# Performance work log

Hardware: AMD Instinct MI355X
Metric: run time of the kernel (lower is better)

## Reference

```python
import jax, jax.numpy as jnp
import numpy as np
import math

B, T, M, C, H = 2, 2048, 1024, 512, 8
D = C // H  # head dim = 64


def setup_inputs() -> dict:
    key = jax.random.key(0)
    ks = jax.random.split(key, 6)
    return {
        "x": jax.random.normal(ks[0], (B, T, C), jnp.float32),
        "y": jax.random.normal(ks[1], (B, M, C), jnp.float32),
        "attn_x_mask": jnp.ones((1, 1, T, T), jnp.int32),
        "qkv_w": jax.random.normal(ks[2], (3 * C, C), jnp.float32) * 0.02,
        "qkv_b": jax.random.normal(ks[3], (3 * C,), jnp.float32) * 0.02,
        "proj_w": jax.random.normal(ks[4], (C, C), jnp.float32) * 0.02,
        "proj_b": jax.random.normal(ks[5], (C,), jnp.float32) * 0.02,
    }


def _split_heads(t, n, d):
    # [B, N, C] -> [B, H, N, D]
    b = t.shape[0]
    return t.reshape(b, n, H, d).transpose(0, 2, 1, 3)


def reference(x, y, attn_x_mask, qkv_w, qkv_b, proj_w, proj_b):
    b, t, c = x.shape
    m = y.shape[1]
    d = c // H
    scale = 1.0 / math.sqrt(d)

    # shared qkv projection applied to x and y (torch Linear: x @ W.T + b)
    qkv_x = x @ qkv_w.T + qkv_b
    q_x, k_x, v_x = jnp.split(qkv_x, 3, axis=-1)
    qkv_y = y @ qkv_w.T + qkv_b
    q_y, k_y, v_y = jnp.split(qkv_y, 3, axis=-1)

    q_x, k_x, v_x = (_split_heads(a, t, d) for a in (q_x, k_x, v_x))
    q_y, k_y, v_y = (_split_heads(a, m, d) for a in (q_y, k_y, v_y))

    # x -> y cross attention scores (pre-softmax, reused for chaining)
    catt_x2y = jnp.einsum("bhtd,bhmd->bhtm", q_x, k_y) * scale  # [B,H,T,M]
    cval_x2y = jnp.einsum("bhtm,bhmd->bhtd", jax.nn.softmax(catt_x2y, axis=-1), v_y)
    cval_x2y = cval_x2y.transpose(0, 2, 1, 3).reshape(b, t, c)

    # y -> x scores, then chained through raw x2y scores
    catt_y2x = jnp.einsum("bhmd,bhsd->bhms", q_y, k_x) * scale  # [B,H,M,T]
    chained = jnp.einsum("bhtm,bhms->bhts", catt_x2y, catt_y2x) * scale  # [B,H,T,T]
    chained = jnp.where(attn_x_mask == 0, -jnp.inf, chained)
    cval_y2x = jnp.einsum("bhts,bhsd->bhtd", jax.nn.softmax(chained, axis=-1), v_x)
    cval_y2x = cval_y2x.transpose(0, 2, 1, 3).reshape(b, t, c)

    out = cval_x2y - cval_y2x
    out = out @ proj_w.T + proj_b  # dropout layers are identity in eval mode
    return out
```

## Files before the change

### kernel.cpp

```cpp
#include <hip/hip_runtime.h>


typedef _Float16 half_t;
typedef _Float16 half8 __attribute__((ext_vector_type(8)));
typedef _Float16 half4v __attribute__((ext_vector_type(4)));
typedef float floatx4 __attribute__((ext_vector_type(4)));
typedef int int4v __attribute__((ext_vector_type(4)));

constexpr int Bc = 2, Tc = 2048, Mc = 1024, Cc = 512, Hc = 8, Dc = 64;
constexpr long BTC = (long)Bc * Tc * Cc;
constexpr long ZT  = (long)Bc * Hc * Tc;
constexpr float S1 = 0.18033688f;

enum { EPI_F16STORE = 0, EPI_QKV_XY = 1, EPI_PROJ = 2 };

struct EpiParams {
  half_t* h0;
  half_t* h1;
  half_t* h2;
  half_t* h3;
  half_t* h4;
  half_t* h5;
  half_t* h6;
  float* f0;
  const float* bias;
  float scale;
  int ldc;
  long bstride;
};

__device__ __forceinline__ void gld_lds16(const half_t* g, half_t* l) {
  __builtin_amdgcn_global_load_lds(
      (const __attribute__((address_space(1))) void*)g,
      (__attribute__((address_space(3))) void*)l, 16, 0, 0);
}

__device__ __forceinline__ int pkrtz(float a, float b) {
  return __builtin_bit_cast(int, __builtin_amdgcn_cvt_pkrtz(a, b));
}
__device__ __forceinline__ void pl16(int& a, int& b) {
  asm volatile("v_permlane16_swap_b32 %0, %1" : "+v"(a), "+v"(b));
}
__device__ __forceinline__ void pl32(int& a, int& b) {
  asm volatile("v_permlane32_swap_b32 %0, %1" : "+v"(a), "+v"(b));
}

template <int BM, int BN, int WMG, int WNG, int EPI>
__global__ __launch_bounds__(256) void gemm_nt(
    const half_t* __restrict__ A, const half_t* __restrict__ Bt,
    int K, int lda, int ldb, long bsA, long bsB, EpiParams ep)
{
  constexpr int BK = 64;
  constexpr int WTM = BM / WMG, WTN = BN / WNG;
  constexpr int MI = WTM / 16, NI = WTN / 16;
  constexpr int AIT = BM * BK / 8 / 256;
  constexpr int BIT = BN * BK / 8 / 256;
  constexpr int NLD = AIT + BIT;
  __shared__ __align__(16) half_t As[2][BM * BK];
  __shared__ __align__(16) half_t Bs[2][BN * BK];

  const int tid = threadIdx.x;
  const int lane = tid & 63;
  const int wave = tid >> 6;
  const int wm = wave / WNG, wn = wave % WNG;
  const int r16 = lane & 15, g = lane >> 4;
  const int z = blockIdx.z;
  const long m0 = (long)blockIdx.y * BM;
  const long n0 = (long)blockIdx.x * BN;
  const half_t* Abase = A + (long)z * bsA + m0 * (long)lda;
  const half_t* Bbase = Bt + (long)z * bsB + n0 * (long)ldb;

  const int rA = wm * WTM + r16;
  const int rB = wn * WTN + r16;

  floatx4 acc[MI][NI];
#pragma unroll
  for (int mi = 0; mi < MI; ++mi)
#pragma unroll
    for (int ni = 0; ni < NI; ++ni)
      acc[mi][ni] = floatx4{0.f, 0.f, 0.f, 0.f};

  auto stage = [&](int kt, int buf) {
#pragma unroll
    for (int i = 0; i < AIT; ++i) {
      const int c = tid + i * 256;
      const int row = c >> 3, js = c & 7;
      const int jg = js ^ (row & 7);
      gld_lds16(Abase + (long)row * lda + kt + jg * 8, &As[buf][c * 8]);
    }
#pragma unroll
    for (int i = 0; i < BIT; ++i) {
      const int c = tid + i * 256;
      const int row = c >> 3, js = c & 7;
      const int jg = js ^ (row & 7);
      gld_lds16(Bbase + (long)row * ldb + kt + jg * 8, &Bs[buf][c * 8]);
    }
  };

  const int NIT = K / BK;
  stage(0, 0);
  asm volatile("" ::: "memory");

  for (int it = 0; it < NIT; ++it) {
    const bool hn = (it + 1 < NIT);
    if (hn) stage((it + 1) * BK, (it + 1) & 1);
    asm volatile("" ::: "memory");
    if (hn) {
      if constexpr (NLD == 6) asm volatile("s_waitcnt vmcnt(6)" ::: "memory");
      else if constexpr (NLD == 4) asm volatile("s_waitcnt vmcnt(4)" ::: "memory");
      else if constexpr (NLD == 8) asm volatile("s_waitcnt vmcnt(8)" ::: "memory");
      else asm volatile("s_waitcnt vmcnt(0)" ::: "memory");
    } else {
      asm volatile("s_waitcnt vmcnt(0)" ::: "memory");
    }
    __builtin_amdgcn_s_barrier();
    asm volatile("" ::: "memory");

    const half_t* Ab = As[it & 1];
    const half_t* Bb = Bs[it & 1];
    half8 aF[MI][2], bF[NI][2];
#pragma unroll
    for (int mi = 0; mi < MI; ++mi)
#pragma unroll
      for (int k2 = 0; k2 < 2; ++k2)
        aF[mi][k2] = *reinterpret_cast<const half8*>(
            &Ab[(rA + mi * 16) * BK + ((k2 * 4 + g) ^ (r16 & 7)) * 8]);
#pragma unroll
    for (int ni = 0; ni < NI; ++ni)
#pragma unroll
      for (int k2 = 0; k2 < 2; ++k2)
        bF[ni][k2] = *reinterpret_cast<const half8*>(
            &Bb[(rB + ni * 16) * BK + ((k2 * 4 + g) ^ (r16 & 7)) * 8]);
    __builtin_amdgcn_s_setprio(1);
#pragma unroll
    for (int k2 = 0; k2 < 2; ++k2)
#pragma unroll
      for (int mi = 0; mi < MI; ++mi)
#pragma unroll
        for (int ni = 0; ni < NI; ++ni)
          acc[mi][ni] = __builtin_amdgcn_mfma_f32_16x16x32_f16(
              aF[mi][k2], bF[ni][k2], acc[mi][ni], 0, 0, 0);
    __builtin_amdgcn_s_setprio(0);
    asm volatile("s_waitcnt lgkmcnt(0)" ::: "memory");
    __builtin_amdgcn_s_barrier();
    asm volatile("" ::: "memory");
  }

#pragma unroll
  for (int mi = 0; mi < MI; ++mi) {
#pragma unroll
    for (int ni = 0; ni < NI; ++ni) {
#pragma unroll
      for (int reg = 0; reg < 4; ++reg) {
        const int r = (int)m0 + wm * WTM + mi * 16 + g * 4 + reg;
        const int c = (int)n0 + wn * WTN + ni * 16 + r16;
        const float v = acc[mi][ni][reg];
        if constexpr (EPI == EPI_F16STORE) {
          ep.h0[(long)z * ep.bstride + (long)r * ep.ldc + c] = (half_t)(v * ep.scale);
        } else if constexpr (EPI == EPI_QKV_XY) {
          const float val = v + ep.bias[c];
          const int which = c >> 9;
          const int cc2 = c & 511;
          const int h = cc2 >> 6, d = cc2 & 63;
          if (r < Bc * Tc) {
            const int b = r >> 11, t = r & (Tc - 1);
            const long bh = (long)(b * Hc + h);
            if (which == 0)      ep.h0[(bh * Tc + t) * Dc + d] = (half_t)(val * S1);
            else if (which == 1) ep.h1[(bh * Tc + t) * Dc + d] = (half_t)val;
            else                 ep.h2[(bh * Dc + d) * Tc + t] = (half_t)val;
          } else {
            const int r2 = r - Bc * Tc;
            const int b = r2 >> 10, t = r2 & (Mc - 1);
            const long bh = (long)(b * Hc + h);
            if (which == 0)      ep.h3[(bh * Dc + d) * Mc + t] = (half_t)(val * 0.125f);
            else if (which == 1) { ep.h4[(bh * Mc + t) * Dc + d] = (half_t)val;
                                   ep.h5[(bh * Dc + d) * Mc + t] = (half_t)val; }
            else                 ep.h6[(bh * Dc + d) * Mc + t] = (half_t)val;
          }
        } else {
          ep.f0[(long)r * Cc + c] = v + ep.bias[c];
        }
      }
    }
  }
}

__global__ __launch_bounds__(256) void wtq2(
    const half_t* __restrict__ QYT, const half_t* __restrict__ KYT,
    const half_t* __restrict__ QX, half_t* __restrict__ Q2)
{
  __shared__ __align__(16) half_t As[2][4096];
  __shared__ __align__(16) half_t Bs[2][4096];
  __shared__ __align__(16) half_t WTs[4096];
  const int tid = threadIdx.x, lane = tid & 63, wave = tid >> 6;
  const int wm = wave >> 1, wn = wave & 1;
  const int r16 = lane & 15, g = lane >> 4;
  const int z = blockIdx.y;
  const int t0 = blockIdx.x * 128;
  const half_t* Aq = QYT + (long)z * Dc * Mc;
  const half_t* Bk = KYT + (long)z * Dc * Mc;

  auto stage1 = [&](int kt, int buf) {
#pragma unroll
    for (int i = 0; i < 2; ++i) {
      const int c = tid + i * 256;
      const int row = c >> 3, js = c & 7, jg = js ^ (row & 7);
      gld_lds16(Aq + (long)row * Mc + kt + jg * 8, &As[buf][c * 8]);
    }
#pragma unroll
    for (int i = 0; i < 2; ++i) {
      const int c = tid + i * 256;
      const int row = c >> 3, js = c & 7, jg = js ^ (row & 7);
      gld_lds16(Bk + (long)row * Mc + kt + jg * 8, &Bs[buf][c * 8]);
    }
  };

  floatx4 acc[2][2];
#pragma unroll
  for (int mi = 0; mi < 2; ++mi)
#pragma unroll
    for (int ni = 0; ni < 2; ++ni) acc[mi][ni] = floatx4{0.f, 0.f, 0.f, 0.f};

  const int rA = wm * 32 + r16, rB = wn * 32 + r16;
  stage1(0, 0);
  asm volatile("" ::: "memory");
  for (int it = 0; it < 16; ++it) {
    const bool hn = (it < 15);
    if (hn) stage1((it + 1) * 64, (it + 1) & 1);
    asm volatile("" ::: "memory");
    if (hn) asm volatile("s_waitcnt vmcnt(4)" ::: "memory");
    else    asm volatile("s_waitcnt vmcnt(0)" ::: "memory");
    __builtin_amdgcn_s_barrier();
    asm volatile("" ::: "memory");
    const half_t* Ab = As[it & 1];
    const half_t* Bb = Bs[it & 1];
    half8 aF[2][2], bF[2][2];
#pragma unroll
    for (int mi = 0; mi < 2; ++mi)
#pragma unroll
      for (int k2 = 0; k2 < 2; ++k2)
        aF[mi][k2] = *reinterpret_cast<const half8*>(
            &Ab[(rA + mi * 16) * 64 + ((k2 * 4 + g) ^ (r16 & 7)) * 8]);
#pragma unroll
    for (int ni = 0; ni < 2; ++ni)
#pragma unroll
      for (int k2 = 0; k2 < 2; ++k2)
        bF[ni][k2] = *reinterpret_cast<const half8*>(
            &Bb[(rB + ni * 16) * 64 + ((k2 * 4 + g) ^ (r16 & 7)) * 8]);
    __builtin_amdgcn_s_setprio(1);
#pragma unroll
    for (int k2 = 0; k2 < 2; ++k2)
#pragma unroll
      for (int mi = 0; mi < 2; ++mi)
#pragma unroll
        for (int ni = 0; ni < 2; ++ni)
          acc[mi][ni] = __builtin_amdgcn_mfma_f32_16x16x32_f16(
              aF[mi][k2], bF[ni][k2], acc[mi][ni], 0, 0, 0);
    __builtin_amdgcn_s_setprio(0);
    asm volatile("s_waitcnt lgkmcnt(0)" ::: "memory");
    __builtin_amdgcn_s_barrier();
    asm volatile("" ::: "memory");
  }

  half_t* P2 = &As[0][0];
#pragma unroll
  for (int i = 0; i < 4; ++i) {
    const int c = tid + i * 256;
    const int row = c >> 3, js = c & 7, jg = js ^ (row & 7);
    gld_lds16(QX + ((long)z * Tc + t0 + row) * 64 + jg * 8, P2 + c * 8);
  }
#pragma unroll
  for (int mi = 0; mi < 2; ++mi)
#pragma unroll
    for (int ni = 0; ni < 2; ++ni)
#pragma unroll
      for (int reg = 0; reg < 4; ++reg) {
        const int r = wm * 32 + mi * 16 + g * 4 + reg;
        const int c = wn * 32 + ni * 16 + r16;
        WTs[r * 64 + (((c >> 3) ^ (r & 7)) << 3) + (c & 7)] =
            (half_t)(acc[mi][ni][reg] * 0.125f);
      }
  __syncthreads();

  floatx4 a2[2][4];
#pragma unroll
  for (int mi = 0; mi < 2; ++mi)
#pragma unroll
    for (int ni = 0; ni < 4; ++ni) a2[mi][ni] = floatx4{0.f, 0.f, 0.f, 0.f};
  const int rA2 = wave * 32 + r16;
  half8 aF2[2][2], bF2[4][2];
#pragma unroll
  for (int mi = 0; mi < 2; ++mi)
#pragma unroll
    for (int k2 = 0; k2 < 2; ++k2)
      aF2[mi][k2] = *reinterpret_cast<const half8*>(
          &P2[(rA2 + mi * 16) * 64 + ((k2 * 4 + g) ^ (r16 & 7)) * 8]);
#pragma unroll
  for (int ni = 0; ni < 4; ++ni)
#pragma unroll
    for (int k2 = 0; k2 < 2; ++k2)
      bF2[ni][k2] = *reinterpret_cast<const half8*>(
          &WTs[(ni * 16 + r16) * 64 + ((k2 * 4 + g) ^ (r16 & 7)) * 8]);
#pragma unroll
  for (int k2 = 0; k2 < 2; ++k2)
#pragma unroll
    for (int mi = 0; mi < 2; ++mi)
#pragma unroll
      for (int ni = 0; ni < 4; ++ni)
        a2[mi][ni] = __builtin_amdgcn_mfma_f32_16x16x32_f16(
            aF2[mi][k2], bF2[ni][k2], a2[mi][ni], 0, 0, 0);
#pragma unroll
  for (int mi = 0; mi < 2; ++mi)
#pragma unroll
    for (int ni = 0; ni < 4; ++ni)
#pragma unroll
      for (int reg = 0; reg < 4; ++reg) {
        const int t = t0 + wave * 32 + mi * 16 + g * 4 + reg;
        const int c = ni * 16 + r16;
        Q2[((long)z * Tc + t) * 64 + c] = (half_t)a2[mi][ni][reg];
      }
}

__device__ __forceinline__ void stageK128(const half_t* Kz, int s0, half_t* dst, int tid) {
#pragma unroll
  for (int i = 0; i < 4; ++i) {
    const int c = tid + i * 256;
    const int row = c >> 3, js = c & 7;
    const int jg = js ^ (row & 7);
    gld_lds16(Kz + (long)(s0 + row) * 64 + jg * 8, dst + c * 8);
  }
}
__device__ __forceinline__ void stageV128(const half_t* Vz, int s0, int Slen, half_t* dst, int tid) {
#pragma unroll
  for (int i = 0; i < 4; ++i) {
    const int c = tid + i * 256;
    const int row = c >> 4, js = c & 15;
    const int jg = js ^ (row & 15);
    gld_lds16(Vz + (long)row * Slen + s0 + jg * 8, dst + c * 8);
  }
}

template <bool MASKED, bool PARTIAL>
__device__ __forceinline__ void flash_body(
    const half_t* __restrict__ Qp, const half_t* __restrict__ Kp,
    const half_t* __restrict__ Vp, const unsigned char* __restrict__ mpk,
    float* __restrict__ PO, float2* __restrict__ ML, half_t* __restrict__ outF,
    int Slen, int sbeg, int scount, int z, int q0,
    half_t* Kb0, half_t* Kb1, half_t* Vb)
{
  const int tid = threadIdx.x, lane = tid & 63, w = tid >> 6;
  const int r16 = lane & 15, g = lane >> 4;
  const int b = z >> 3, h = z & 7;
  const int NT = Slen >> 7;
  const half_t* Qz = Qp + ((long)z * Tc + q0) * 64;
  const half_t* Kz = Kp + (long)z * Slen * 64;
  const half_t* Vz = Vp + (long)z * 64 * Slen;

  stageK128(Kz, sbeg, Kb0, tid);
  asm volatile("" ::: "memory");
  stageV128(Vz, sbeg, Slen, Vb, tid);
  asm volatile("" ::: "memory");

  half8 aQ[2][2];
#pragma unroll
  for (int mi = 0; mi < 2; ++mi)
#pragma unroll
    for (int k2 = 0; k2 < 2; ++k2)
      aQ[mi][k2] = *reinterpret_cast<const half8*>(
          Qz + (w * 32 + mi * 16 + r16) * 64 + k2 * 32 + g * 8);

  floatx4 oaccT[2][4];
  float lrun[2];
#pragma unroll
  for (int mi = 0; mi < 2; ++mi) {
    lrun[mi] = 0.f;
#pragma unroll
    for (int no = 0; no < 4; ++no) oaccT[mi][no] = floatx4{0.f, 0.f, 0.f, 0.f};
  }

  const int send = sbeg + scount;
  int cur = 0;
  for (int s0 = sbeg; s0 < send; s0 += 128) {
    const bool hn = (s0 + 128 < send);
    asm volatile("s_waitcnt vmcnt(4)" ::: "memory");
    __builtin_amdgcn_s_barrier();
    asm volatile("" ::: "memory");

    unsigned int mb32[2];
    if constexpr (MASKED) {
      const int tile = s0 >> 7;
#pragma unroll
      for (int mi = 0; mi < 2; ++mi) {
        const int q = q0 + w * 32 + mi * 16 + r16;
        mb32[mi] = *reinterpret_cast<const unsigned int*>(
            mpk + ((long)q * NT + tile) * 16 + 4 * g);
      }
    }

    floatx4 sacc[2][8];
#pragma unroll
    for (int mi = 0; mi < 2; ++mi)
#pragma unroll
      for (int ni = 0; ni < 8; ++ni) sacc[mi][ni] = floatx4{0.f, 0.f, 0.f, 0.f};
    const half_t* Kc = cur ? Kb1 : Kb0;
    __builtin_amdgcn_s_setprio(1);
#pragma unroll
    for (int ni = 0; ni < 8; ++ni) {
      const int rB = ni * 16 + r16;
      const half8 b0 = *reinterpret_cast<const half8*>(&Kc[rB * 64 + (g ^ (rB & 7)) * 8]);
      const half8 b1 = *reinterpret_cast<const half8*>(&Kc[rB * 64 + ((4 + g) ^ (rB & 7)) * 8]);
#pragma unroll
      for (int mi = 0; mi < 2; ++mi) {
        sacc[mi][ni] = __builtin_amdgcn_mfma_f32_16x16x32_f16(b0, aQ[mi][0], sacc[mi][ni], 0, 0, 0);
        sacc[mi][ni] = __builtin_amdgcn_mfma_f32_16x16x32_f16(b1, aQ[mi][1], sacc[mi][ni], 0, 0, 0);
      }
    }
    __builtin_amdgcn_s_setprio(0);
    if (hn) stageK128(Kz, s0 + 128, cur ? Kb0 : Kb1, tid);
    asm volatile("" ::: "memory");

#pragma unroll
    for (int mi = 0; mi < 2; ++mi) {
      if constexpr (MASKED) {
        if (mb32[mi] != 0xffffffffu) {
#pragma unroll
          for (int reg = 0; reg < 4; ++reg)
#pragma unroll
            for (int ni = 0; ni < 8; ++ni)
              if (!((mb32[mi] >> (reg * 8 + ni)) & 1)) sacc[mi][ni][reg] = -__builtin_inff();
        }
      }
      float ls = 0.f;
#pragma unroll
      for (int ni = 0; ni < 8; ++ni)
#pragma unroll
        for (int reg = 0; reg < 4; ++reg) {
          const float e = __builtin_amdgcn_exp2f(sacc[mi][ni][reg]);
          sacc[mi][ni][reg] = e;
          ls += e;
        }
      ls += __shfl_xor(ls, 16);
      ls += __shfl_xor(ls, 32);
      lrun[mi] += ls;
    }

    if (hn) { asm volatile("s_waitcnt vmcnt(4)" ::: "memory"); }
    else    { asm volatile("s_waitcnt vmcnt(0)" ::: "memory"); }
    __builtin_amdgcn_s_barrier();
    asm volatile("" ::: "memory");

#pragma unroll
    for (int c = 0; c < 4; ++c) {
      half8 bVv[4];
#pragma unroll
      for (int no = 0; no < 4; ++no) {
        const int rV = no * 16 + r16;
        bVv[no] = *reinterpret_cast<const half8*>(
            &Vb[rV * 128 + ((c * 4 + g) ^ (rV & 15)) * 8]);
      }
#pragma unroll
      for (int mi = 0; mi < 2; ++mi) {
        int x0 = pkrtz(sacc[mi][2 * c][0],     sacc[mi][2 * c][1]);
        int x1 = pkrtz(sacc[mi][2 * c][2],     sacc[mi][2 * c][3]);
        int x2 = pkrtz(sacc[mi][2 * c + 1][0], sacc[mi][2 * c + 1][1]);
        int x3 = pkrtz(sacc[mi][2 * c + 1][2], sacc[mi][2 * c + 1][3]);
        pl32(x0, x2); pl32(x1, x3);
        pl16(x0, x2); pl16(x1, x3);
        int4v wv; wv[0] = x0; wv[1] = x1; wv[2] = x2; wv[3] = x3;
        const half8 aP = __builtin_bit_cast(half8, wv);
        __builtin_amdgcn_s_setprio(1);
#pragma unroll
        for (int no = 0; no < 4; ++no)
          oaccT[mi][no] = __builtin_amdgcn_mfma_f32_16x16x32_f16(bVv[no], aP, oaccT[mi][no], 0, 0, 0);
        __builtin_amdgcn_s_setprio(0);
      }
    }
    __builtin_amdgcn_s_barrier();
    asm volatile("" ::: "memory");
    if (hn) stageV128(Vz, s0 + 128, Slen, Vb, tid);
    asm volatile("" ::: "memory");
    cur ^= 1;
  }

  float* slab = reinterpret_cast<float*>(Vb) + w * 1024;
#pragma unroll
  for (int mi = 0; mi < 2; ++mi) {
    const int tq = q0 + w * 32 + mi * 16;
    if constexpr (PARTIAL) {
      if (lane < 16)
        ML[(long)z * Tc + tq + r16] = float2{0.f, lrun[mi]};
    }
    const float sc = PARTIAL ? 1.f : (1.f / lrun[mi]);
#pragma unroll
    for (int no = 0; no < 4; ++no) {
      floatx4 v = oaccT[mi][no];
      if constexpr (!PARTIAL) v *= sc;
      *reinterpret_cast<floatx4*>(&slab[r16 * 64 + no * 16 + (g ^ (r16 & 3)) * 4]) = v;
    }
#pragma unroll
    for (int it = 0; it < 4; ++it) {
      const int q2 = it * 4 + g;
      const int d4 = r16;
      const floatx4 v = *reinterpret_cast<const floatx4*>(
          &slab[q2 * 64 + (d4 >> 2) * 16 + ((d4 & 3) ^ (q2 & 3)) * 4]);
      const long off = ((long)(b * Tc + tq + q2)) * Cc + h * 64 + d4 * 4;
      if constexpr (PARTIAL) {
        *reinterpret_cast<floatx4*>(&PO[off]) = v;
      } else {
        half4v hh; hh[0] = (half_t)v[0]; hh[1] = (half_t)v[1];
        hh[2] = (half_t)v[2]; hh[3] = (half_t)v[3];
        *reinterpret_cast<half4v*>(&outF[off]) = hh;
      }
    }
  }
}

__global__ __launch_bounds__(256, 3) void flash_both(
    const half_t* __restrict__ Q2, const half_t* __restrict__ KX,
    const half_t* __restrict__ VXT, const unsigned char* __restrict__ mpk,
    const half_t* __restrict__ QX, const half_t* __restrict__ KY,
    const half_t* __restrict__ VYT,
    float* __restrict__ PO, float2* __restrict__ ML, half_t* __restrict__ DH2)
{
  __shared__ __align__(16) half_t Kb0[8192];
  __shared__ __align__(16) half_t Kb1[8192];
  __shared__ __align__(16) half_t Vb[8192];
  const int bx = blockIdx.x;
  if (bx < 512) {
    const int z  = ((bx & 7) << 1) | ((bx >> 3) & 1);
    const int sh = (bx >> 4) & 1;
    const int q0 = (bx >> 5) * 128;
    flash_body<true, true>(Q2, KX, VXT, mpk,
                           PO + (long)sh * BTC, ML + (long)sh * ZT, nullptr,
                           Tc, sh * 1024, 1024, z, q0, Kb0, Kb1, Vb);
  } else {
    const int b2 = bx - 512;
    const int z  = ((b2 & 7) << 1) | ((b2 >> 3) & 1);
    const int q0 = (b2 >> 4) * 128;
    flash_body<false, false>(QX, KY, VYT, nullptr,
                             nullptr, nullptr, DH2,
                             Mc, 0, Mc, z, q0, Kb0, Kb1, Vb);
  }
}

__global__ __launch_bounds__(256) void combine_k(
    const float* __restrict__ PO, const float2* __restrict__ ML,
    const half_t* __restrict__ DH2, half_t* __restrict__ DH)
{
  const long idx = (long)blockIdx.x * 256 + threadIdx.x;
  const long c4 = idx * 4;
  const int c = (int)(c4 & (Cc - 1));
  const long bt = c4 >> 9;
  const int h = c >> 6;
  const int b = (int)(bt >> 11), t = (int)(bt & (Tc - 1));
  const long zt = (long)(b * Hc + h) * Tc + t;
  const float2 a0 = ML[zt], a1 = ML[ZT + zt];
  const float ainv = 1.f / (a0.y + a1.y);
  const float4* PO4 = reinterpret_cast<const float4*>(PO);
  const float4 oa0 = PO4[idx];
  const float4 oa1 = PO4[BTC / 4 + idx];
  const half4v dv = reinterpret_cast<const half4v*>(DH2)[idx];
  half4v r;
  r[0] = (half_t)((float)dv[0] - (oa0.x + oa1.x) * ainv);
  r[1] = (half_t)((float)dv[1] - (oa0.y + oa1.y) * ainv);
  r[2] = (half_t)((float)dv[2] - (oa0.z + oa1.z) * ainv);
  r[3] = (half_t)((float)dv[3] - (oa0.w + oa1.w) * ainv);
  reinterpret_cast<half4v*>(DH)[idx] = r;
}

__device__ __forceinline__ void cvt4(const float* in, half_t* out, long i) {
  const float4 f = reinterpret_cast<const float4*>(in)[i];
  half4v h; h[0] = (half_t)f.x; h[1] = (half_t)f.y; h[2] = (half_t)f.z; h[3] = (half_t)f.w;
  reinterpret_cast<half4v*>(out)[i] = h;
}

__global__ __launch_bounds__(256) void prep(
    const float* __restrict__ x, const float* __restrict__ y,
    const float* __restrict__ qw, const float* __restrict__ pw,
    const int* __restrict__ mask,
    half_t* __restrict__ XH, half_t* __restrict__ YH,
    half_t* __restrict__ WQ, half_t* __restrict__ WP,
    unsigned char* __restrict__ mpk)
{
  const long i = (long)blockIdx.x * 256 + threadIdx.x;
  constexpr long n0 = 524288;
  constexpr long n1 = n0 + 262144;
  constexpr long n2 = n1 + 196608;
  constexpr long n3 = n2 + 65536;
  if (i < n0) cvt4(x, XH, i);
  else if (i < n1) cvt4(y, YH, i - n0);
  else if (i < n2) cvt4(qw, WQ, i - n1);
  else if (i < n3) cvt4(pw, WP, i - n2);
  else {
    const long idx = i - n3;
    const int t = (int)(idx >> 8), tile = (int)((idx >> 4) & 15), r16 = (int)(idx & 15);
    const int* row = mask + (long)t * Tc + tile * 128 + r16;
    unsigned int bbits = 0;
#pragma unroll
    for (int ni = 0; ni < 8; ++ni)
      bbits |= (row[ni * 16] != 0 ? 1u : 0u) << ni;
    mpk[idx] = (unsigned char)bbits;
  }
}

constexpr size_t OFF_XH   = 0;
constexpr size_t OFF_YH   = OFF_XH   + (size_t)Bc*Tc*Cc*2;
constexpr size_t OFF_WQ   = OFF_YH   + (size_t)Bc*Mc*Cc*2;
constexpr size_t OFF_WP   = OFF_WQ   + (size_t)3*Cc*Cc*2;
constexpr size_t OFF_QX   = OFF_WP   + (size_t)Cc*Cc*2;
constexpr size_t OFF_KX   = OFF_QX   + (size_t)Bc*Hc*Tc*Dc*2;
constexpr size_t OFF_VXT  = OFF_KX   + (size_t)Bc*Hc*Tc*Dc*2;
constexpr size_t OFF_QYT  = OFF_VXT  + (size_t)Bc*Hc*Tc*Dc*2;
constexpr size_t OFF_KY   = OFF_QYT  + (size_t)Bc*Hc*Mc*Dc*2;
constexpr size_t OFF_KYT  = OFF_KY   + (size_t)Bc*Hc*Mc*Dc*2;
constexpr size_t OFF_VYT  = OFF_KYT  + (size_t)Bc*Hc*Mc*Dc*2;
constexpr size_t OFF_WT   = OFF_VYT  + (size_t)Bc*Hc*Mc*Dc*2;
constexpr size_t OFF_Q2   = OFF_WT   + (size_t)Bc*Hc*Dc*Dc*2;
constexpr size_t OFF_DH   = OFF_Q2   + (size_t)Bc*Hc*Tc*Dc*2;
constexpr size_t OFF_DH2  = OFF_DH   + (size_t)Bc*Tc*Cc*2;
constexpr size_t OFF_MPK  = OFF_DH2  + (size_t)Bc*Tc*Cc*2;
constexpr size_t OFF_PO   = OFF_MPK  + (size_t)Tc*256;
constexpr size_t OFF_ML   = OFF_PO   + (size_t)2*BTC*4;

extern "C" void kernel_launch(void* const* d_in, const int* in_sizes, int n_in,
                              void* d_out, int out_size, void* d_ws, size_t ws_size,
                              hipStream_t stream) {
  const float* x      = (const float*)d_in[0];
  const float* y      = (const float*)d_in[1];
  const int*   mask   = (const int*)  d_in[2];
  const float* qkv_b  = (const float*)d_in[4];
  const float* proj_b = (const float*)d_in[6];
  float* out = (float*)d_out;
  char* ws = (char*)d_ws;

  half_t* XH   = (half_t*)(ws + OFF_XH);
  half_t* YH   = (half_t*)(ws + OFF_YH);
  half_t* WQ   = (half_t*)(ws + OFF_WQ);
  half_t* WP   = (half_t*)(ws + OFF_WP);
  half_t* QX   = (half_t*)(ws + OFF_QX);
  half_t* KX   = (half_t*)(ws + OFF_KX);
  half_t* VXT  = (half_t*)(ws + OFF_VXT);
  half_t* QYT  = (half_t*)(ws + OFF_QYT);
  half_t* KY   = (half_t*)(ws + OFF_KY);
  half_t* KYT  = (half_t*)(ws + OFF_KYT);
  half_t* VYT  = (half_t*)(ws + OFF_VYT);
  half_t* Q2   = (half_t*)(ws + OFF_Q2);
  half_t* DH   = (half_t*)(ws + OFF_DH);
  half_t* DH2  = (half_t*)(ws + OFF_DH2);
  unsigned char* MPK = (unsigned char*)(ws + OFF_MPK);
  float*  PO   = (float*) (ws + OFF_PO);
  float2* ML   = (float2*)(ws + OFF_ML);

  prep<<<6144, 256, 0, stream>>>(x, y, (const float*)d_in[3], (const float*)d_in[5],
                                 mask, XH, YH, WQ, WP, MPK);

  {
    EpiParams ep{};
    ep.h0 = QX; ep.h1 = KX; ep.h2 = VXT; ep.h3 = QYT;
    ep.h4 = KY; ep.h5 = KYT; ep.h6 = VYT; ep.bias = qkv_b;
    gemm_nt<128,64,2,2,EPI_QKV_XY><<<dim3(24, 48, 1), 256, 0, stream>>>(
        XH, WQ, Cc, Cc, Cc, 0, 0, ep);
  }

  wtq2<<<dim3(16, 16), 256, 0, stream>>>(QYT, KYT, QX, Q2);

  flash_both<<<dim3(768), 256, 0, stream>>>(
      Q2, KX, VXT, MPK, QX, KY, VYT, PO, ML, DH2);

  combine_k<<<(int)(BTC/4/256), 256, 0, stream>>>(PO, ML, DH2, DH);

  {
    EpiParams ep{}; ep.f0 = out; ep.bias = proj_b;
    gemm_nt<64,64,2,2,EPI_PROJ><<<dim3(8, 64, 1), 256, 0, stream>>>(
        DH, WP, Cc, Cc, Cc, 0, 0, ep);
  }
}
```

Before: 175.4 us.

## Drop split-S flash partials, double-buffer V, fuse combine into projection GEMM

The chained-attention flash blocks now cover the full 2048-key range instead of two split halves, so the partial-sum ML buffer and the separate combine kernel go away. The subtraction DH2 - PO is folded into a new projection GEMM that loads both operands and converts to fp16 on the fly. The flash loop now double-buffers V alongside K with a single barrier per tile and defers the row-sum shuffle reduction to the end. The trade-off is fewer blocks (512 instead of 768), which lowers parallelism, and a 2-block occupancy bound because of the larger LDS footprint.

```diff
diff --git a/kernel.cpp b/kernel.cpp
--- a/kernel.cpp
+++ b/kernel.cpp
@@ -9,7 +9,6 @@
 
 constexpr int Bc = 2, Tc = 2048, Mc = 1024, Cc = 512, Hc = 8, Dc = 64;
 constexpr long BTC = (long)Bc * Tc * Cc;
-constexpr long ZT  = (long)Bc * Hc * Tc;
 constexpr float S1 = 0.18033688f;
 
 enum { EPI_F16STORE = 0, EPI_QKV_XY = 1, EPI_PROJ = 2 };
@@ -340,13 +339,13 @@
   }
 }
 
-template <bool MASKED, bool PARTIAL>
+template <bool MASKED, bool F32OUT>
 __device__ __forceinline__ void flash_body(
     const half_t* __restrict__ Qp, const half_t* __restrict__ Kp,
     const half_t* __restrict__ Vp, const unsigned char* __restrict__ mpk,
-    float* __restrict__ PO, float2* __restrict__ ML, half_t* __restrict__ outF,
-    int Slen, int sbeg, int scount, int z, int q0,
-    half_t* Kb0, half_t* Kb1, half_t* Vb)
+    float* __restrict__ PO, half_t* __restrict__ outF,
+    int Slen, int scount, int z, int q0,
+    half_t* Kb0, half_t* Kb1, half_t* Vb0, half_t* Vb1)
 {
   const int tid = threadIdx.x, lane = tid & 63, w = tid >> 6;
   const int r16 = lane & 15, g = lane >> 4;
@@ -356,9 +355,8 @@
   const half_t* Kz = Kp + (long)z * Slen * 64;
   const half_t* Vz = Vp + (long)z * 64 * Slen;
 
-  stageK128(Kz, sbeg, Kb0, tid);
-  asm volatile("" ::: "memory");
-  stageV128(Vz, sbeg, Slen, Vb, tid);
+  stageK128(Kz, 0, Kb0, tid);
+  stageV128(Vz, 0, Slen, Vb0, tid);
   asm volatile("" ::: "memory");
 
   half8 aQ[2][2];
@@ -370,30 +368,34 @@
           Qz + (w * 32 + mi * 16 + r16) * 64 + k2 * 32 + g * 8);
 
   floatx4 oaccT[2][4];
-  float lrun[2];
+  float lsum[2];
 #pragma unroll
   for (int mi = 0; mi < 2; ++mi) {
-    lrun[mi] = 0.f;
+    lsum[mi] = 0.f;
 #pragma unroll
     for (int no = 0; no < 4; ++no) oaccT[mi][no] = floatx4{0.f, 0.f, 0.f, 0.f};
   }
 
-  const int send = sbeg + scount;
-  int cur = 0;
-  for (int s0 = sbeg; s0 < send; s0 += 128) {
-    const bool hn = (s0 + 128 < send);
-    asm volatile("s_waitcnt vmcnt(4)" ::: "memory");
+  const int nt = scount >> 7;
+  for (int t = 0; t < nt; ++t) {
+    const bool hn = (t + 1 < nt);
+    const int s0 = t << 7;
+    asm volatile("s_waitcnt vmcnt(0)" ::: "memory");
     __builtin_amdgcn_s_barrier();
+    asm volatile("" ::: "memory");
+    if (hn) {
+      stageK128(Kz, s0 + 128, (t & 1) ? Kb0 : Kb1, tid);
+      stageV128(Vz, s0 + 128, Slen, (t & 1) ? Vb0 : Vb1, tid);
+    }
     asm volatile("" ::: "memory");
 
     unsigned int mb32[2];
     if constexpr (MASKED) {
-      const int tile = s0 >> 7;
 #pragma unroll
       for (int mi = 0; mi < 2; ++mi) {
         const int q = q0 + w * 32 + mi * 16 + r16;
         mb32[mi] = *reinterpret_cast<const unsigned int*>(
-            mpk + ((long)q * NT + tile) * 16 + 4 * g);
+            mpk + ((long)q * NT + t) * 16 + 4 * g);
       }
     }
 
@@ -402,7 +404,8 @@
     for (int mi = 0; mi < 2; ++mi)
 #pragma unroll
       for (int ni = 0; ni < 8; ++ni) sacc[mi][ni] = floatx4{0.f, 0.f, 0.f, 0.f};
-    const half_t* Kc = cur ? Kb1 : Kb0;
+    const half_t* Kc = (t & 1) ? Kb1 : Kb0;
+    const half_t* Vc = (t & 1) ? Vb1 : Vb0;
     __builtin_amdgcn_s_setprio(1);
 #pragma unroll
     for (int ni = 0; ni < 8; ++ni) {
@@ -416,47 +419,35 @@
       }
     }
     __builtin_amdgcn_s_setprio(0);
-    if (hn) stageK128(Kz, s0 + 128, cur ? Kb0 : Kb1, tid);
-    asm volatile("" ::: "memory");
-
-#pragma unroll
-    for (int mi = 0; mi < 2; ++mi) {
-      if constexpr (MASKED) {
-        if (mb32[mi] != 0xffffffffu) {
-#pragma unroll
-          for (int reg = 0; reg < 4; ++reg)
-#pragma unroll
-            for (int ni = 0; ni < 8; ++ni)
-              if (!((mb32[mi] >> (reg * 8 + ni)) & 1)) sacc[mi][ni][reg] = -__builtin_inff();
+
+#pragma unroll
+    for (int c = 0; c < 4; ++c) {
+#pragma unroll
+      for (int mi = 0; mi < 2; ++mi) {
+#pragma unroll
+        for (int hf = 0; hf < 2; ++hf) {
+          const int ni = 2 * c + hf;
+          if constexpr (MASKED) {
+            if (mb32[mi] != 0xffffffffu) {
+#pragma unroll
+              for (int reg = 0; reg < 4; ++reg)
+                if (!((mb32[mi] >> (reg * 8 + ni)) & 1)) sacc[mi][ni][reg] = -__builtin_inff();
+            }
+          }
+#pragma unroll
+          for (int reg = 0; reg < 4; ++reg) {
+            const float e = __builtin_amdgcn_exp2f(sacc[mi][ni][reg]);
+            sacc[mi][ni][reg] = e;
+            lsum[mi] += e;
+          }
         }
       }
-      float ls = 0.f;
-#pragma unroll
-      for (int ni = 0; ni < 8; ++ni)
-#pragma unroll
-        for (int reg = 0; reg < 4; ++reg) {
-          const float e = __builtin_amdgcn_exp2f(sacc[mi][ni][reg]);
-          sacc[mi][ni][reg] = e;
-          ls += e;
-        }
-      ls += __shfl_xor(ls, 16);
-      ls += __shfl_xor(ls, 32);
-      lrun[mi] += ls;
-    }
-
-    if (hn) { asm volatile("s_waitcnt vmcnt(4)" ::: "memory"); }
-    else    { asm volatile("s_waitcnt vmcnt(0)" ::: "memory"); }
-    __builtin_amdgcn_s_barrier();
-    asm volatile("" ::: "memory");
-
-#pragma unroll
-    for (int c = 0; c < 4; ++c) {
       half8 bVv[4];
 #pragma unroll
       for (int no = 0; no < 4; ++no) {
         const int rV = no * 16 + r16;
         bVv[no] = *reinterpret_cast<const half8*>(
-            &Vb[rV * 128 + ((c * 4 + g) ^ (rV & 15)) * 8]);
+            &Vc[rV * 128 + ((c * 4 + g) ^ (rV & 15)) * 8]);
       }
 #pragma unroll
       for (int mi = 0; mi < 2; ++mi) {
@@ -475,26 +466,23 @@
         __builtin_amdgcn_s_setprio(0);
       }
     }
-    __builtin_amdgcn_s_barrier();
-    asm volatile("" ::: "memory");
-    if (hn) stageV128(Vz, s0 + 128, Slen, Vb, tid);
-    asm volatile("" ::: "memory");
-    cur ^= 1;
-  }
-
-  float* slab = reinterpret_cast<float*>(Vb) + w * 1024;
+  }
+
+  float lr[2];
+#pragma unroll
+  for (int mi = 0; mi < 2; ++mi) {
+    float ls = lsum[mi];
+    ls += __shfl_xor(ls, 16);
+    ls += __shfl_xor(ls, 32);
+    lr[mi] = 1.f / ls;
+  }
+  float* slab = reinterpret_cast<float*>(Vb0) + w * 1024;
 #pragma unroll
   for (int mi = 0; mi < 2; ++mi) {
     const int tq = q0 + w * 32 + mi * 16;
-    if constexpr (PARTIAL) {
-      if (lane < 16)
-        ML[(long)z * Tc + tq + r16] = float2{0.f, lrun[mi]};
-    }
-    const float sc = PARTIAL ? 1.f : (1.f / lrun[mi]);
 #pragma unroll
     for (int no = 0; no < 4; ++no) {
-      floatx4 v = oaccT[mi][no];
-      if constexpr (!PARTIAL) v *= sc;
+      floatx4 v = oaccT[mi][no] * lr[mi];
       *reinterpret_cast<floatx4*>(&slab[r16 * 64 + no * 16 + (g ^ (r16 & 3)) * 4]) = v;
     }
 #pragma unroll
@@ -504,7 +492,7 @@
       const floatx4 v = *reinterpret_cast<const floatx4*>(
           &slab[q2 * 64 + (d4 >> 2) * 16 + ((d4 & 3) ^ (q2 & 3)) * 4]);
       const long off = ((long)(b * Tc + tq + q2)) * Cc + h * 64 + d4 * 4;
-      if constexpr (PARTIAL) {
+      if constexpr (F32OUT) {
         *reinterpret_cast<floatx4*>(&PO[off]) = v;
       } else {
         half4v hh; hh[0] = (half_t)v[0]; hh[1] = (half_t)v[1];
@@ -515,57 +503,141 @@
   }
 }
 
-__global__ __launch_bounds__(256, 3) void flash_both(
+__global__ __launch_bounds__(256, 2) void flash_both(
     const half_t* __restrict__ Q2, const half_t* __restrict__ KX,
     const half_t* __restrict__ VXT, const unsigned char* __restrict__ mpk,
     const half_t* __restrict__ QX, const half_t* __restrict__ KY,
     const half_t* __restrict__ VYT,
-    float* __restrict__ PO, float2* __restrict__ ML, half_t* __restrict__ DH2)
+    float* __restrict__ PO, half_t* __restrict__ DH2)
 {
   __shared__ __align__(16) half_t Kb0[8192];
   __shared__ __align__(16) half_t Kb1[8192];
-  __shared__ __align__(16) half_t Vb[8192];
+  __shared__ __align__(16) half_t Vb0[8192];
+  __shared__ __align__(16) half_t Vb1[8192];
   const int bx = blockIdx.x;
-  if (bx < 512) {
+  if (bx < 256) {
     const int z  = ((bx & 7) << 1) | ((bx >> 3) & 1);
-    const int sh = (bx >> 4) & 1;
-    const int q0 = (bx >> 5) * 128;
-    flash_body<true, true>(Q2, KX, VXT, mpk,
-                           PO + (long)sh * BTC, ML + (long)sh * ZT, nullptr,
-                           Tc, sh * 1024, 1024, z, q0, Kb0, Kb1, Vb);
+    const int q0 = (bx >> 4) * 128;
+    flash_body<true, true>(Q2, KX, VXT, mpk, PO, nullptr,
+                           Tc, Tc, z, q0, Kb0, Kb1, Vb0, Vb1);
   } else {
-    const int b2 = bx - 512;
+    const int b2 = bx - 256;
     const int z  = ((b2 & 7) << 1) | ((b2 >> 3) & 1);
     const int q0 = (b2 >> 4) * 128;
-    flash_body<false, false>(QX, KY, VYT, nullptr,
-                             nullptr, nullptr, DH2,
-                             Mc, 0, Mc, z, q0, Kb0, Kb1, Vb);
-  }
-}
-
-__global__ __launch_bounds__(256) void combine_k(
-    const float* __restrict__ PO, const float2* __restrict__ ML,
-    const half_t* __restrict__ DH2, half_t* __restrict__ DH)
+    flash_body<false, false>(QX, KY, VYT, nullptr, nullptr, DH2,
+                             Mc, Mc, z, q0, Kb0, Kb1, Vb0, Vb1);
+  }
+}
+
+__global__ __launch_bounds__(256) void gemm_proj(
+    const half_t* __restrict__ DH2, const float* __restrict__ PO,
+    const half_t* __restrict__ WP, const float* __restrict__ bias,
+    float* __restrict__ out)
 {
-  const long idx = (long)blockIdx.x * 256 + threadIdx.x;
-  const long c4 = idx * 4;
-  const int c = (int)(c4 & (Cc - 1));
-  const long bt = c4 >> 9;
-  const int h = c >> 6;
-  const int b = (int)(bt >> 11), t = (int)(bt & (Tc - 1));
-  const long zt = (long)(b * Hc + h) * Tc + t;
-  const float2 a0 = ML[zt], a1 = ML[ZT + zt];
-  const float ainv = 1.f / (a0.y + a1.y);
-  const float4* PO4 = reinterpret_cast<const float4*>(PO);
-  const float4 oa0 = PO4[idx];
-  const float4 oa1 = PO4[BTC / 4 + idx];
-  const half4v dv = reinterpret_cast<const half4v*>(DH2)[idx];
-  half4v r;
-  r[0] = (half_t)((float)dv[0] - (oa0.x + oa1.x) * ainv);
-  r[1] = (half_t)((float)dv[1] - (oa0.y + oa1.y) * ainv);
-  r[2] = (half_t)((float)dv[2] - (oa0.z + oa1.z) * ainv);
-  r[3] = (half_t)((float)dv[3] - (oa0.w + oa1.w) * ainv);
-  reinterpret_cast<half4v*>(DH)[idx] = r;
+  constexpr int BK = 64, NIT = 8;
+  __shared__ __align__(16) half_t As[2][64 * 64];
+  __shared__ __align__(16) half_t Bs[2][64 * 64];
+  const int tid = threadIdx.x, lane = tid & 63, wave = tid >> 6;
+  const int wm = wave >> 1, wn = wave & 1;
+  const int r16 = lane & 15, g = lane >> 4;
+  const long m0 = (long)blockIdx.y * 64;
+  const long n0 = (long)blockIdx.x * 64;
+
+  half8  a_d2[2][2];
+  float4 a_po[2][2][2];
+
+  auto issueA = [&](int kt, int buf) {
+#pragma unroll
+    for (int i = 0; i < 2; ++i) {
+      const int c = tid + i * 256;
+      const int row = c >> 3, js = c & 7, jg = js ^ (row & 7);
+      const long off = (m0 + row) * Cc + kt + jg * 8;
+      a_d2[buf][i] = *reinterpret_cast<const half8*>(&DH2[off]);
+      a_po[buf][i][0] = *reinterpret_cast<const float4*>(&PO[off]);
+      a_po[buf][i][1] = *reinterpret_cast<const float4*>(&PO[off + 4]);
+    }
+  };
+  auto issueB = [&](int kt, int buf) {
+#pragma unroll
+    for (int i = 0; i < 2; ++i) {
+      const int c = tid + i * 256;
+      const int row = c >> 3, js = c & 7, jg = js ^ (row & 7);
+      gld_lds16(WP + (n0 + row) * Cc + kt + jg * 8, &Bs[buf][c * 8]);
+    }
+  };
+
+  floatx4 acc[2][2];
+#pragma unroll
+  for (int mi = 0; mi < 2; ++mi)
+#pragma unroll
+    for (int ni = 0; ni < 2; ++ni) acc[mi][ni] = floatx4{0.f, 0.f, 0.f, 0.f};
+
+  const int rA = wm * 32 + r16, rB = wn * 32 + r16;
+
+  issueA(0, 0); issueB(0, 0);
+  asm volatile("" ::: "memory");
+
+#pragma unroll
+  for (int t = 0; t < NIT; ++t) {
+    const bool hn = (t + 1 < NIT);
+    if (hn) { issueA((t + 1) * BK, (t + 1) & 1); issueB((t + 1) * BK, (t + 1) & 1); }
+    asm volatile("" ::: "memory");
+    if (hn) asm volatile("s_waitcnt vmcnt(8)" ::: "memory");
+    else    asm volatile("s_waitcnt vmcnt(0)" ::: "memory");
+#pragma unroll
+    for (int i = 0; i < 2; ++i) {
+      const int c = tid + i * 256;
+      const float4 p0 = a_po[t & 1][i][0], p1 = a_po[t & 1][i][1];
+      const half8 d2 = a_d2[t & 1][i];
+      int w0 = pkrtz((float)d2[0] - p0.x, (float)d2[1] - p0.y);
+      int w1 = pkrtz((float)d2[2] - p0.z, (float)d2[3] - p0.w);
+      int w2 = pkrtz((float)d2[4] - p1.x, (float)d2[5] - p1.y);
+      int w3 = pkrtz((float)d2[6] - p1.z, (float)d2[7] - p1.w);
+      int4v wv; wv[0] = w0; wv[1] = w1; wv[2] = w2; wv[3] = w3;
+      *reinterpret_cast<int4v*>(&As[t & 1][c * 8]) = wv;
+    }
+    asm volatile("s_waitcnt lgkmcnt(0)" ::: "memory");
+    __builtin_amdgcn_s_barrier();
+    asm volatile("" ::: "memory");
+
+    half8 aF[2][2], bF[2][2];
+#pragma unroll
+    for (int mi = 0; mi < 2; ++mi)
+#pragma unroll
+      for (int k2 = 0; k2 < 2; ++k2)
+        aF[mi][k2] = *reinterpret_cast<const half8*>(
+            &As[t & 1][(rA + mi * 16) * BK + ((k2 * 4 + g) ^ (r16 & 7)) * 8]);
+#pragma unroll
+    for (int ni = 0; ni < 2; ++ni)
+#pragma unroll
+      for (int k2 = 0; k2 < 2; ++k2)
+        bF[ni][k2] = *reinterpret_cast<const half8*>(
+            &Bs[t & 1][(rB + ni * 16) * BK + ((k2 * 4 + g) ^ (r16 & 7)) * 8]);
+    __builtin_amdgcn_s_setprio(1);
+#pragma unroll
+    for (int k2 = 0; k2 < 2; ++k2)
+#pragma unroll
+      for (int mi = 0; mi < 2; ++mi)
+#pragma unroll
+        for (int ni = 0; ni < 2; ++ni)
+          acc[mi][ni] = __builtin_amdgcn_mfma_f32_16x16x32_f16(
+              aF[mi][k2], bF[ni][k2], acc[mi][ni], 0, 0, 0);
+    __builtin_amdgcn_s_setprio(0);
+    asm volatile("s_waitcnt lgkmcnt(0)" ::: "memory");
+    __builtin_amdgcn_s_barrier();
+    asm volatile("" ::: "memory");
+  }
+
+#pragma unroll
+  for (int mi = 0; mi < 2; ++mi)
+#pragma unroll
+    for (int ni = 0; ni < 2; ++ni)
+#pragma unroll
+      for (int reg = 0; reg < 4; ++reg) {
+        const long r = m0 + wm * 32 + mi * 16 + g * 4 + reg;
+        const int  c = (int)n0 + wn * 32 + ni * 16 + r16;
+        out[r * Cc + c] = acc[mi][ni][reg] + bias[c];
+      }
 }
 
 __device__ __forceinline__ void cvt4(const float* in, half_t* out, long i) {
@@ -614,13 +686,10 @@
 constexpr size_t OFF_KY   = OFF_QYT  + (size_t)Bc*Hc*Mc*Dc*2;
 constexpr size_t OFF_KYT  = OFF_KY   + (size_t)Bc*Hc*Mc*Dc*2;
 constexpr size_t OFF_VYT  = OFF_KYT  + (size_t)Bc*Hc*Mc*Dc*2;
-constexpr size_t OFF_WT   = OFF_VYT  + (size_t)Bc*Hc*Mc*Dc*2;
-constexpr size_t OFF_Q2   = OFF_WT   + (size_t)Bc*Hc*Dc*Dc*2;
-constexpr size_t OFF_DH   = OFF_Q2   + (size_t)Bc*Hc*Tc*Dc*2;
-constexpr size_t OFF_DH2  = OFF_DH   + (size_t)Bc*Tc*Cc*2;
+constexpr size_t OFF_Q2   = OFF_VYT  + (size_t)Bc*Hc*Mc*Dc*2;
+constexpr size_t OFF_DH2  = OFF_Q2   + (size_t)Bc*Hc*Tc*Dc*2;
 constexpr size_t OFF_MPK  = OFF_DH2  + (size_t)Bc*Tc*Cc*2;
 constexpr size_t OFF_PO   = OFF_MPK  + (size_t)Tc*256;
-constexpr size_t OFF_ML   = OFF_PO   + (size_t)2*BTC*4;
 
 extern "C" void kernel_launch(void* const* d_in, const int* in_sizes, int n_in,
                               void* d_out, int out_size, void* d_ws, size_t ws_size,
@@ -645,11 +714,9 @@
   half_t* KYT  = (half_t*)(ws + OFF_KYT);
   half_t* VYT  = (half_t*)(ws + OFF_VYT);
   half_t* Q2   = (half_t*)(ws + OFF_Q2);
-  half_t* DH   = (half_t*)(ws + OFF_DH);
   half_t* DH2  = (half_t*)(ws + OFF_DH2);
   unsigned char* MPK = (unsigned char*)(ws + OFF_MPK);
   float*  PO   = (float*) (ws + OFF_PO);
-  float2* ML   = (float2*)(ws + OFF_ML);
 
   prep<<<6144, 256, 0, stream>>>(x, y, (const float*)d_in[3], (const float*)d_in[5],
                                  mask, XH, YH, WQ, WP, MPK);
@@ -664,14 +731,8 @@
 
   wtq2<<<dim3(16, 16), 256, 0, stream>>>(QYT, KYT, QX, Q2);
 
-  flash_both<<<dim3(768), 256, 0, stream>>>(
-      Q2, KX, VXT, MPK, QX, KY, VYT, PO, ML, DH2);
-
-  combine_k<<<(int)(BTC/4/256), 256, 0, stream>>>(PO, ML, DH2, DH);
-
-  {
-    EpiParams ep{}; ep.f0 = out; ep.bias = proj_b;
-    gemm_nt<64,64,2,2,EPI_PROJ><<<dim3(8, 64, 1), 256, 0, stream>>>(
-        DH, WP, Cc, Cc, Cc, 0, 0, ep);
-  }
-}
+  flash_both<<<dim3(512), 256, 0, stream>>>(
+      Q2, KX, VXT, MPK, QX, KY, VYT, PO, DH2);
+
+  gemm_proj<<<dim3(8, 64), 256, 0, stream>>>(DH2, PO, WP, proj_b, out);
+}
```

After: 183.6 us. +4.6%, slower.
